# Optimization experiments

Hardware: AMD Instinct MI355X
Metric: run time of the kernel (lower is better)

Reference implementation:

```python
import jax, jax.numpy as jnp
import numpy as np

B, N, C, H = 8, 1024, 512, 8
EPS = 1e-6


def setup_inputs() -> dict:
    key = jax.random.key(0)
    k0, k1, k2, k3, k4 = jax.random.split(key, 5)
    x = jax.random.normal(k0, (B, N, C), dtype=jnp.float32)
    # nonnegative random-walk visit-frequency mask stand-in
    mask = jax.random.uniform(k1, (N, N), dtype=jnp.float32)
    w_qkv = jax.random.normal(k2, (C, 3 * C), dtype=jnp.float32) * 0.02
    w_out = jax.random.normal(k3, (C, C), dtype=jnp.float32) * 0.02
    b_out = jax.random.normal(k4, (C,), dtype=jnp.float32) * 0.02
    return {"x": x, "mask": mask, "w_qkv": w_qkv, "w_out": w_out, "b_out": b_out}


def reference(x, mask, w_qkv, w_out, b_out):
    b, n, c = x.shape
    d = c // H
    qkv = x @ w_qkv                                   # [B,N,3C]
    q, k, v = jnp.split(qkv, 3, axis=-1)

    def to_heads(t):
        return t.reshape(b, n, H, d).transpose(0, 2, 1, 3)  # [B,H,N,D]

    q, k, v = to_heads(q), to_heads(k), to_heads(v)
    # positive feature map
    q = jax.nn.relu(q) + EPS
    k = jax.nn.relu(k) + EPS
    # graph diffusion: (q^T @ mask)^T == einsum over source node m
    q = q + 0.1 * jnp.einsum('bhmd,mn->bhnd', q, mask)
    k = k + 0.1 * jnp.einsum('bhmd,mn->bhnd', k, mask)
    # linear kernel scores, elementwise-masked
    kernel = jnp.einsum('bhnd,bhmd->bhnm', q, k) * mask   # [B,H,N,N]
    z = 1.0 / (kernel.sum(axis=-1, keepdims=True) + EPS)  # [B,H,N,1]
    out = jnp.einsum('bhnm,bhmd->bhnd', kernel, v) * z    # [B,H,N,D]
    out = out.transpose(0, 2, 1, 3).reshape(b, n, c)      # [B,N,C]
    return out @ w_out + b_out
```

## Files before the change

### kernel.cpp

```cpp
#include <hip/hip_runtime.h>
#include <cstddef>

#define Bsz 8
#define Nn  1024
#define Cc  512
#define Hh  8
#define Dd  64
#define EPSF 1e-6f

typedef __attribute__((ext_vector_type(8))) short short8;
typedef __attribute__((ext_vector_type(4))) float floatx4;

static __device__ __forceinline__ short f2bf(float f) {
    union { float f; unsigned u; } v; v.f = f;
    unsigned r = (v.u + 0x7FFFu + ((v.u >> 16) & 1u)) >> 16;
    return (short)r;
}
static __device__ __forceinline__ float bf2f(short s) {
    union { unsigned u; float f; } v; v.u = ((unsigned)(unsigned short)s) << 16;
    return v.f;
}

#define GLOAD_LDS16(gp, lp)                                              \
    __builtin_amdgcn_global_load_lds(                                    \
        (const __attribute__((address_space(1))) void*)(gp),             \
        (__attribute__((address_space(3))) void*)(lp), 16, 0, 0)

static __device__ __forceinline__
void stage_tile(short* __restrict__ lds, const short* __restrict__ src,
                int ldsrc, int tid, int CHUNKS, int SLOTS) {
    #pragma unroll
    for (int s = tid; s < SLOTS; s += 256) {
        int r = s / CHUNKS, cs = s % CHUNKS;
        int gc = cs ^ (r & 7);
        GLOAD_LDS16(&src[(size_t)r * ldsrc + gc * 8], &lds[s * 8]);
    }
}
static __device__ __forceinline__
short8 fragT(const short* __restrict__ lds, int CHUNKS, int r, int lc) {
    return *(const short8*)&lds[(r * CHUNKS + (lc ^ (r & 7))) * 8];
}

#define FENCE() asm volatile("" ::: "memory")
#define BARRIER_RAW() do { FENCE(); __builtin_amdgcn_s_barrier(); FENCE(); } while (0)
#define WAITVM(N) asm volatile("s_waitcnt vmcnt(" #N ")" ::: "memory")

__global__ __launch_bounds__(256)
void prep_all(const float* __restrict__ x, const float* __restrict__ mask,
              const float* __restrict__ wq, const float* __restrict__ wo,
              short* __restrict__ xb, short* __restrict__ Ad,
              short* __restrict__ wqT, short* __restrict__ woT,
              short* __restrict__ mbf) {
    __shared__ float t[64][65];
    const int tid = threadIdx.x;
    const int bid = blockIdx.x;

    if (bid < 2048) {
        int idx = bid * 256 + tid;
        const float* s = &x[(size_t)idx * 8];
        union { short h[8]; int4 v; } u;
        #pragma unroll
        for (int j = 0; j < 8; j++) u.h[j] = f2bf(s[j]);
        *(int4*)&xb[(size_t)idx * 8] = u.v;
        return;
    }
    if (bid < 2304) {
        int idx = bid - 2048;
        const int n0 = (idx & 15) * 64, m0 = (idx >> 4) * 64;
        #pragma unroll
        for (int i = 0; i < 4; i++) {
            int k = i * 256 + tid;
            int r = k >> 4, c4 = (k & 15) * 4;
            *(float4*)&t[r][c4] = *(const float4*)&mask[(size_t)(m0 + r) * Nn + n0 + c4];
        }
        __syncthreads();
        #pragma unroll
        for (int i = 0; i < 4; i++) {
            int k = i * 256 + tid;
            int rr = k >> 4, c4 = (k & 15) * 4;
            union { short h[4]; int2 v; } u;
            #pragma unroll
            for (int j = 0; j < 4; j++) {
                int mm = c4 + j;
                float v = 0.1f * t[mm][rr] + ((n0 + rr) == (m0 + mm) ? 1.0f : 0.0f);
                u.h[j] = f2bf(v);
            }
            *(int2*)&Ad[(size_t)(n0 + rr) * Nn + m0 + c4] = u.v;
        }
        return;
    }
    if (bid < 2496) {
        int idx = bid - 2304;
        const int n0 = (idx % 24) * 64, k0 = (idx / 24) * 64;
        #pragma unroll
        for (int i = 0; i < 4; i++) {
            int k = i * 256 + tid;
            int r = k >> 4, c4 = (k & 15) * 4;
            *(float4*)&t[r][c4] = *(const float4*)&wq[(size_t)(k0 + r) * 1536 + n0 + c4];
        }
        __syncthreads();
        #pragma unroll
        for (int i = 0; i < 4; i++) {
            int k = i * 256 + tid;
            int rr = k >> 4, c4 = (k & 15) * 4;
            union { short h[4]; int2 v; } u;
            #pragma unroll
            for (int j = 0; j < 4; j++) u.h[j] = f2bf(t[c4 + j][rr]);
            *(int2*)&wqT[(size_t)(n0 + rr) * 512 + k0 + c4] = u.v;
        }
        return;
    }
    if (bid < 2560) {
        int idx = bid - 2496;
        const int n0 = (idx & 7) * 64, k0 = (idx >> 3) * 64;
        #pragma unroll
        for (int i = 0; i < 4; i++) {
            int k = i * 256 + tid;
            int r = k >> 4, c4 = (k & 15) * 4;
            *(float4*)&t[r][c4] = *(const float4*)&wo[(size_t)(k0 + r) * 512 + n0 + c4];
        }
        __syncthreads();
        #pragma unroll
        for (int i = 0; i < 4; i++) {
            int k = i * 256 + tid;
            int rr = k >> 4, c4 = (k & 15) * 4;
            union { short h[4]; int2 v; } u;
            #pragma unroll
            for (int j = 0; j < 4; j++) u.h[j] = f2bf(t[c4 + j][rr]);
            *(int2*)&woT[(size_t)(n0 + rr) * 512 + k0 + c4] = u.v;
        }
        return;
    }
    {
        int idx = (bid - 2560) * 256 + tid;
        const float* s = &mask[(size_t)idx * 8];
        union { short h[8]; int4 v; } u;
        #pragma unroll
        for (int j = 0; j < 8; j++) u.h[j] = f2bf(s[j]);
        *(int4*)&mbf[(size_t)idx * 8] = u.v;
    }
}

static __device__ __forceinline__
void stageA_half(short* __restrict__ buf, const short* __restrict__ gA,
                 int kt, int h, int tid) {
    #pragma unroll
    for (int kk = 0; kk < 2; kk++) {
        int i = tid + kk * 512;
        int run = i >> 9;
        int within = i & 511;
        int r = run * 128 + h * 64 + (within >> 3);
        int c = within & 7;
        int gc = c ^ (r & 7);
        GLOAD_LDS16(gA + (size_t)r * 512 + kt + gc * 8, buf + (r * 8 + c) * 8);
    }
}
static __device__ __forceinline__
void stageB_half(short* __restrict__ buf, const short* __restrict__ gB,
                 int kt, int h, int tid) {
    #pragma unroll
    for (int kk = 0; kk < 2; kk++) {
        int i = tid + kk * 512;
        int run = i >> 8;
        int within = i & 255;
        int r = run * 64 + h * 32 + (within >> 3);
        int c = within & 7;
        int gc = c ^ (r & 7);
        GLOAD_LDS16(gB + (size_t)r * 512 + kt + gc * 8, buf + (r * 8 + c) * 8);
    }
}

template<int MH>
static __device__ __forceinline__
void readA8(const short* __restrict__ bufA, short8 (&aF)[4][2],
            int wr, int l16, int quad) {
    #pragma unroll
    for (int f = 0; f < 4; f++)
        #pragma unroll
        for (int kk = 0; kk < 2; kk++)
            aF[f][kk] = fragT(bufA, 8, wr * 128 + MH * 64 + f * 16 + l16, kk * 4 + quad);
}
template<int NH>
static __device__ __forceinline__
void readB4(const short* __restrict__ bufB, short8 (&bF)[2][2],
            int wc, int l16, int quad) {
    #pragma unroll
    for (int g = 0; g < 2; g++)
        #pragma unroll
        for (int kk = 0; kk < 2; kk++)
            bF[g][kk] = fragT(bufB, 8, wc * 64 + NH * 32 + g * 16 + l16, kk * 4 + quad);
}
template<int MH, int NH>
static __device__ __forceinline__
void mfma16(short8 (&aF)[4][2], short8 (&bF)[2][2], floatx4 (&acc)[8][4]) {
    #pragma unroll
    for (int kk = 0; kk < 2; kk++)
        #pragma unroll
        for (int f = 0; f < 4; f++)
            #pragma unroll
            for (int g = 0; g < 2; g++)
                acc[MH * 4 + f][NH * 2 + g] = __builtin_amdgcn_mfma_f32_16x16x32_bf16(
                    aF[f][kk], bF[g][kk], acc[MH * 4 + f][NH * 2 + g], 0, 0, 0);
}

__global__ __launch_bounds__(512, 2)
void gemm_qkv(const short* __restrict__ xb, const short* __restrict__ wqT,
              short* __restrict__ qT, short* __restrict__ kT,
              short* __restrict__ vT) {
    extern __shared__ short smem[];

    const int tid = threadIdx.x;
    const int lin = blockIdx.x;
    const int wgid = (lin & 7) * 24 + (lin >> 3);
    const int mt = wgid / 6, nt = wgid % 6;
    const int m0 = mt * 256, n0 = nt * 256;

    const int wid = tid >> 6, lane = tid & 63;
    const int quad = lane >> 4, l16 = lane & 15;
    const int wr = wid >> 2, wc = wid & 3;

    const short* Ab = xb  + (size_t)m0 * 512;
    const short* Bb = wqT + (size_t)n0 * 512;

    floatx4 acc[8][4];
    #pragma unroll
    for (int i = 0; i < 8; i++)
        #pragma unroll
        for (int j = 0; j < 4; j++) acc[i][j] = (floatx4){0.f, 0.f, 0.f, 0.f};

    short8 aF[4][2], bF[2][2];

    stageA_half(smem,          Ab, 0, 0, tid);
    stageB_half(smem + 16384,  Bb, 0, 0, tid);
    stageA_half(smem,          Ab, 0, 1, tid);
    stageB_half(smem + 16384,  Bb, 0, 1, tid);
    WAITVM(4); BARRIER_RAW();

    for (int j = 0; j < 8; ++j) {
        const short* cA = smem + (j & 1) * 32768;
        const short* cB = cA + 16384;
        short* nA = smem + ((j + 1) & 1) * 32768;
        short* nB = nA + 16384;
        const int kn = ((j + 1) & 7) * 64;

        readA8<0>(cA, aF, wr, l16, quad);
        readB4<0>(cB, bF, wc, l16, quad);
        stageA_half(nA, Ab, kn, 0, tid);
        stageB_half(nB, Bb, kn, 0, tid);
        BARRIER_RAW();
        __builtin_amdgcn_s_setprio(1);
        mfma16<0, 0>(aF, bF, acc);
        __builtin_amdgcn_s_setprio(0);
        WAITVM(4); BARRIER_RAW();

        readA8<1>(cA, aF, wr, l16, quad);
        stageA_half(nA, Ab, kn, 1, tid);
        stageB_half(nB, Bb, kn, 1, tid);
        BARRIER_RAW();
        __builtin_amdgcn_s_setprio(1);
        mfma16<1, 0>(aF, bF, acc);
        __builtin_amdgcn_s_setprio(0);
        BARRIER_RAW();

        readB4<1>(cB, bF, wc, l16, quad);
        BARRIER_RAW();
        __builtin_amdgcn_s_setprio(1);
        mfma16<1, 1>(aF, bF, acc);
        __builtin_amdgcn_s_setprio(0);
        BARRIER_RAW();

        readA8<0>(cA, aF, wr, l16, quad);
        BARRIER_RAW();
        __builtin_amdgcn_s_setprio(1);
        mfma16<0, 1>(aF, bF, acc);
        __builtin_amdgcn_s_setprio(0);
        WAITVM(4); BARRIER_RAW();
    }

    WAITVM(0); BARRIER_RAW();

    short* T = smem + wid * 8192;
    const int doRelu = (n0 < 1024);
    #pragma unroll
    for (int mf = 0; mf < 8; mf++)
        #pragma unroll
        for (int nf = 0; nf < 4; nf++)
            #pragma unroll
            for (int rr = 0; rr < 4; rr++) {
                float v = acc[mf][nf][rr];
                if (doRelu) v = fmaxf(v, 0.0f) + EPSF;
                int row = nf * 16 + l16;
                int col = mf * 16 + quad * 4 + rr;
                T[row * 128 + (col ^ ((row & 15) << 3))] = f2bf(v);
            }
    const int gm0 = m0 + wr * 128;
    const int b = gm0 >> 10, m_in0 = gm0 & 1023;
    #pragma unroll
    for (int g = 0; g < 4; g++) {
        int row = (lane >> 2) + g * 16;
        int gn = n0 + wc * 64 + row;
        int part = gn >> 9, ci = gn & 511;
        short* base = (part == 0) ? qT : (part == 1) ? kT : vT;
        short* dst = base + ((size_t)b * 512 + ci) * 1024 + m_in0;
        #pragma unroll
        for (int cc = 0; cc < 4; cc++) {
            int cs = ((lane & 3) + cc * 4) * 8;
            *(int4*)&dst[cs] = *(const int4*)&T[row * 128 + (cs ^ ((row & 15) << 3))];
        }
    }
}

static __device__ __forceinline__
void dstageA_half(short* __restrict__ buf, const short* __restrict__ gA,
                  int kt, int h, int tid) {
    #pragma unroll
    for (int kk = 0; kk < 2; kk++) {
        int i = tid + kk * 512;
        int rl = i >> 3;
        int c  = i & 7;
        int r  = (rl >> 5) * 64 + h * 32 + (rl & 31);
        int gc = c ^ (r & 7);
        GLOAD_LDS16(gA + (size_t)r * 1024 + kt + gc * 8, buf + (r * 8 + c) * 8);
    }
}
static __device__ __forceinline__
void dstageB_half(short* __restrict__ buf, const short* __restrict__ gB,
                  int kt, int h, int tid) {
    int rl = tid >> 3;
    int c  = tid & 7;
    int r  = (rl >> 5) * 64 + h * 32 + (rl & 31);
    int gc = c ^ (r & 7);
    GLOAD_LDS16(gB + (size_t)r * 1024 + kt + gc * 8, buf + (r * 8 + c) * 8);
}
template<int MH>
static __device__ __forceinline__
void dreadA(const short* __restrict__ bufA, short8 (&aF)[2][2],
            int wr, int l16, int quad) {
    #pragma unroll
    for (int f = 0; f < 2; f++)
        #pragma unroll
        for (int kk = 0; kk < 2; kk++)
            aF[f][kk] = fragT(bufA, 8, wr * 64 + MH * 32 + f * 16 + l16, kk * 4 + quad);
}
template<int NH>
static __device__ __forceinline__
void dreadB(const short* __restrict__ bufB, short8 (&bF)[2][2],
            int wc, int l16, int quad) {
    #pragma unroll
    for (int g = 0; g < 2; g++)
        #pragma unroll
        for (int kk = 0; kk < 2; kk++)
            bF[g][kk] = fragT(bufB, 8, wc * 64 + NH * 32 + g * 16 + l16, kk * 4 + quad);
}
template<int MH, int NH>
static __device__ __forceinline__
void dmfma8(short8 (&aF)[2][2], short8 (&bF)[2][2], floatx4 (&acc)[4][4]) {
    #pragma unroll
    for (int kk = 0; kk < 2; kk++)
        #pragma unroll
        for (int f = 0; f < 2; f++)
            #pragma unroll
            for (int g = 0; g < 2; g++)
                acc[MH * 2 + f][NH * 2 + g] = __builtin_amdgcn_mfma_f32_16x16x32_bf16(
                    aF[f][kk], bF[g][kk], acc[MH * 2 + f][NH * 2 + g], 0, 0, 0);
}

__global__ __launch_bounds__(512, 2)
void gemm_diff8(const short* __restrict__ Ad, const short* __restrict__ qT,
                const short* __restrict__ kT, short* __restrict__ qd,
                short* __restrict__ kd) {
    extern __shared__ short smem[];

    const int tid = threadIdx.x;
    const int lin = blockIdx.x;
    const int wgid = (lin & 7) * 32 + (lin >> 3);
    const int mt = wgid >> 6, ct = wgid & 63;
    const int m0 = mt * 256;
    const int seg = ct >> 2, cb = (ct & 3) * 128;
    const int b = seg >> 1, part = seg & 1;

    const short* Bb = ((part ? kT : qT) + (size_t)b * 512 * 1024) + (size_t)cb * 1024;
    short* outb = (part ? kd : qd) + (size_t)b * 1024 * 512;
    const short* Abase = Ad + (size_t)m0 * 1024;

    const int wid = tid >> 6, lane = tid & 63;
    const int quad = lane >> 4, l16 = lane & 15;
    const int wr = wid >> 1, wc = wid & 1;

    floatx4 acc[4][4];
    #pragma unroll
    for (int i = 0; i < 4; i++)
        #pragma unroll
        for (int j = 0; j < 4; j++) acc[i][j] = (floatx4){0.f, 0.f, 0.f, 0.f};

    short8 aF[2][2], bF[2][2];

    dstageA_half(smem,          Abase, 0, 0, tid);
    dstageB_half(smem + 16384,  Bb,    0, 0, tid);
    dstageA_half(smem,          Abase, 0, 1, tid);
    dstageB_half(smem + 16384,  Bb,    0, 1, tid);
    WAITVM(3); BARRIER_RAW();

    for (int j = 0; j < 16; ++j) {
        const short* cA = smem + (j & 1) * 24576;
        const short* cB = cA + 16384;
        short* nA = smem + ((j + 1) & 1) * 24576;
        short* nB = nA + 16384;
        const int kn = ((j + 1) & 15) * 64;

        dreadA<0>(cA, aF, wr, l16, quad);
        dreadB<0>(cB, bF, wc, l16, quad);
        dstageA_half(nA, Abase, kn, 0, tid);
        dstageB_half(nB, Bb,    kn, 0, tid);
        BARRIER_RAW();
        __builtin_amdgcn_s_setprio(1);
        dmfma8<0, 0>(aF, bF, acc);
        __builtin_amdgcn_s_setprio(0);
        WAITVM(3); BARRIER_RAW();

        dreadA<1>(cA, aF, wr, l16, quad);
        dstageA_half(nA, Abase, kn, 1, tid);
        dstageB_half(nB, Bb,    kn, 1, tid);
        BARRIER_RAW();
        __builtin_amdgcn_s_setprio(1);
        dmfma8<1, 0>(aF, bF, acc);
        __builtin_amdgcn_s_setprio(0);
        BARRIER_RAW();

        dreadB<1>(cB, bF, wc, l16, quad);
        BARRIER_RAW();
        __builtin_amdgcn_s_setprio(1);
        dmfma8<1, 1>(aF, bF, acc);
        __builtin_amdgcn_s_setprio(0);
        BARRIER_RAW();

        dreadA<0>(cA, aF, wr, l16, quad);
        BARRIER_RAW();
        __builtin_amdgcn_s_setprio(1);
        dmfma8<0, 1>(aF, bF, acc);
        __builtin_amdgcn_s_setprio(0);
        WAITVM(3); BARRIER_RAW();
    }
    WAITVM(0);

    #pragma unroll
    for (int fr = 0; fr < 4; fr++)
        #pragma unroll
        for (int rr = 0; rr < 4; rr++) {
            int n = m0 + wr * 64 + fr * 16 + quad * 4 + rr;
            #pragma unroll
            for (int fc = 0; fc < 4; fc++) {
                int c = cb + wc * 64 + fc * 16 + l16;
                outb[(size_t)n * 512 + c] = f2bf(acc[fr][fc][rr]);
            }
        }
}

static __device__ __forceinline__
void attn_tile(const short* __restrict__ ks, const short* __restrict__ vt,
               short* __restrict__ ss, const int2 (&M)[2][4],
               const short8 (&aT)[2][2], float (&dreg)[2],
               floatx4 (&nacc)[2][4], int wave, int quad, int l16) {
    const int ssrow[2] = { wave * 32 + l16, wave * 32 + 16 + l16 };
    #pragma unroll
    for (int mt = 0; mt < 4; mt++) {
        const short8 k0f = fragT(ks, 8, mt * 16 + l16, quad);
        const short8 k1f = fragT(ks, 8, mt * 16 + l16, 4 + quad);
        #pragma unroll
        for (int t = 0; t < 2; t++) {
            floatx4 s = (floatx4){0.f, 0.f, 0.f, 0.f};
            s = __builtin_amdgcn_mfma_f32_16x16x32_bf16(k0f, aT[t][0], s, 0, 0, 0);
            s = __builtin_amdgcn_mfma_f32_16x16x32_bf16(k1f, aT[t][1], s, 0, 0, 0);
            const int row = ssrow[t];
            const int c = mt * 16 + quad * 4;
            const int off = (row * 8 + ((c >> 3) ^ (row & 7))) * 8 + (c & 7);
            union { short hh[4]; int2 v; } mk; mk.v = M[t][mt];
            float sv0 = s[0] * bf2f(mk.hh[0]);
            float sv1 = s[1] * bf2f(mk.hh[1]);
            float sv2 = s[2] * bf2f(mk.hh[2]);
            float sv3 = s[3] * bf2f(mk.hh[3]);
            dreg[t] += (sv0 + sv1) + (sv2 + sv3);
            int lo, hi;
            asm("v_cvt_pk_bf16_f32 %0, %1, %2" : "=v"(lo) : "v"(sv0), "v"(sv1));
            asm("v_cvt_pk_bf16_f32 %0, %1, %2" : "=v"(hi) : "v"(sv2), "v"(sv3));
            int2 pv; pv.x = lo; pv.y = hi;
            *(int2*)&ss[off] = pv;
        }
    }
    short8 p[2][2];
    #pragma unroll
    for (int t = 0; t < 2; t++) {
        p[t][0] = fragT(ss, 8, wave * 32 + t * 16 + l16, quad);
        p[t][1] = fragT(ss, 8, wave * 32 + t * 16 + l16, 4 + quad);
    }
    __builtin_amdgcn_s_setprio(1);
    #pragma unroll
    for (int dt = 0; dt < 4; dt++) {
        const short8 v0 = fragT(vt, 8, dt * 16 + l16, quad);
        const short8 v1 = fragT(vt, 8, dt * 16 + l16, 4 + quad);
        #pragma unroll
        for (int t = 0; t < 2; t++) {
            nacc[t][dt] = __builtin_amdgcn_mfma_f32_16x16x32_bf16(p[t][0], v0, nacc[t][dt], 0, 0, 0);
            nacc[t][dt] = __builtin_amdgcn_mfma_f32_16x16x32_bf16(p[t][1], v1, nacc[t][dt], 0, 0, 0);
        }
    }
    __builtin_amdgcn_s_setprio(0);
}

__global__ __launch_bounds__(256)
void attn_mfma(const short* __restrict__ qd, const short* __restrict__ kd,
               const short* __restrict__ vTg, const short* __restrict__ mbf,
               short* __restrict__ abf) {
    __shared__ short qss[8192];
    __shared__ short kv[2][8192];

    const int tid = threadIdx.x;
    const int bh = blockIdx.x;
    const int b = bh >> 3, h = bh & 7;
    const int n0 = blockIdx.y * 128;

    const int wave = tid >> 6, lane = tid & 63;
    const int quad = lane >> 4, l16 = lane & 15;

    const short* Qb = qd + ((size_t)b * Nn + n0) * Cc + h * Dd;
    const short* Kb = kd + (size_t)b * Nn * Cc + h * Dd;
    const short* Vb = vTg + ((size_t)b * Cc + h * Dd) * Nn;
    const short* baseM = mbf + (size_t)(n0 + wave * 32 + l16) * Nn + quad * 4;

    stage_tile(qss, Qb, Cc, tid, 8, 1024);
    stage_tile(kv[0],        Kb, Cc, tid, 8, 512);
    stage_tile(kv[0] + 4096, Vb, Nn, tid, 8, 512);
    int2 Ma[2][4], Mb2[2][4];
    #pragma unroll
    for (int t = 0; t < 2; t++)
        #pragma unroll
        for (int mt = 0; mt < 4; mt++)
            Ma[t][mt] = *(const int2*)(baseM + t * 16 * Nn + mt * 16);
    WAITVM(0); BARRIER_RAW();

    short8 aT[2][2];
    #pragma unroll
    for (int t = 0; t < 2; t++) {
        aT[t][0] = fragT(qss, 8, wave * 32 + t * 16 + l16, quad);
        aT[t][1] = fragT(qss, 8, wave * 32 + t * 16 + l16, 4 + quad);
    }

    float dreg[2] = {0.f, 0.f};
    floatx4 nacc[2][4];
    #pragma unroll
    for (int t = 0; t < 2; t++)
        #pragma unroll
        for (int i = 0; i < 4; i++) nacc[t][i] = (floatx4){0.f, 0.f, 0.f, 0.f};

    for (int jo = 0; jo < 8; jo++) {
        const int j0 = jo * 2;
        stage_tile(kv[1],        Kb + (size_t)(j0 + 1) * 64 * Cc, Cc, tid, 8, 512);
        stage_tile(kv[1] + 4096, Vb + (j0 + 1) * 64,              Nn, tid, 8, 512);
        #pragma unroll
        for (int t = 0; t < 2; t++)
            #pragma unroll
            for (int mt = 0; mt < 4; mt++)
                Mb2[t][mt] = *(const int2*)(baseM + t * 16 * Nn + (j0 + 1) * 64 + mt * 16);
        attn_tile(kv[0], kv[0] + 4096, qss, Ma, aT, dreg, nacc, wave, quad, l16);
        WAITVM(0); BARRIER_RAW();

        if (jo < 7) {
            stage_tile(kv[0],        Kb + (size_t)(j0 + 2) * 64 * Cc, Cc, tid, 8, 512);
            stage_tile(kv[0] + 4096, Vb + (j0 + 2) * 64,              Nn, tid, 8, 512);
            #pragma unroll
            for (int t = 0; t < 2; t++)
                #pragma unroll
                for (int mt = 0; mt < 4; mt++)
                    Ma[t][mt] = *(const int2*)(baseM + t * 16 * Nn + (j0 + 2) * 64 + mt * 16);
        }
        attn_tile(kv[1], kv[1] + 4096, qss, Mb2, aT, dreg, nacc, wave, quad, l16);
        WAITVM(0); BARRIER_RAW();
    }

    #pragma unroll
    for (int t = 0; t < 2; t++) {
        dreg[t] += __shfl_xor(dreg[t], 16, 64);
        dreg[t] += __shfl_xor(dreg[t], 32, 64);
    }

    #pragma unroll
    for (int t = 0; t < 2; t++)
        #pragma unroll
        for (int r = 0; r < 4; r++) {
            int nloc = quad * 4 + r;
            float den = __shfl(dreg[t], nloc, 64);
            int n = n0 + wave * 32 + t * 16 + nloc;
            float zr = 1.0f / (den + EPSF);
            #pragma unroll
            for (int dt = 0; dt < 4; dt++) {
                size_t o = ((size_t)b * Nn + n) * Cc + h * Dd + dt * 16 + l16;
                abf[o] = f2bf(nacc[t][dt][r] * zr);
            }
        }
}

__global__ __launch_bounds__(256)
void gemm_out(const short* __restrict__ abf, const short* __restrict__ woT,
              const float* __restrict__ bias, float* __restrict__ out) {
    __shared__ short smem[12288];
    short* As = smem;
    short* Bs = smem + 4096;

    const int tid = threadIdx.x;
    const int m0 = blockIdx.y * 64;
    const int n0 = blockIdx.x * 128;
    const int wave = tid >> 6, lane = tid & 63;
    const int quad = lane >> 4, l16 = lane & 15;
    const int wm = (wave >> 1) * 32, wn = (wave & 1) * 64;

    floatx4 acc[2][4];
    #pragma unroll
    for (int i = 0; i < 2; i++)
        #pragma unroll
        for (int j = 0; j < 4; j++) acc[i][j] = (floatx4){0.f, 0.f, 0.f, 0.f};

    const short* Ab = abf + (size_t)m0 * 512;
    const short* Bb = woT + (size_t)n0 * 512;

    for (int k0 = 0; k0 < 512; k0 += 64) {
        __syncthreads();
        stage_tile(As, Ab + k0, 512, tid, 8, 512);
        stage_tile(Bs, Bb + k0, 512, tid, 8, 1024);
        __syncthreads();
        #pragma unroll
        for (int kh = 0; kh < 2; kh++) {
            short8 a[2], b[4];
            #pragma unroll
            for (int i = 0; i < 2; i++)
                a[i] = fragT(As, 8, wm + i * 16 + l16, kh * 4 + quad);
            #pragma unroll
            for (int i = 0; i < 4; i++)
                b[i] = fragT(Bs, 8, wn + i * 16 + l16, kh * 4 + quad);
            #pragma unroll
            for (int mi = 0; mi < 2; mi++)
                #pragma unroll
                for (int ni = 0; ni < 4; ni++)
                    acc[mi][ni] = __builtin_amdgcn_mfma_f32_16x16x32_bf16(
                        a[mi], b[ni], acc[mi][ni], 0, 0, 0);
        }
    }

    #pragma unroll
    for (int mi = 0; mi < 2; mi++)
        #pragma unroll
        for (int r = 0; r < 4; r++) {
            int m = m0 + wm + mi * 16 + quad * 4 + r;
            #pragma unroll
            for (int ni = 0; ni < 4; ni++) {
                int n = n0 + wn + ni * 16 + l16;
                out[(size_t)m * 512 + n] = acc[mi][ni][r] + bias[n];
            }
        }
}

extern "C" void kernel_launch(void* const* d_in, const int* in_sizes, int n_in,
                              void* d_out, int out_size, void* d_ws, size_t ws_size,
                              hipStream_t stream) {
    const float* x     = (const float*)d_in[0];
    const float* mask  = (const float*)d_in[1];
    const float* w_qkv = (const float*)d_in[2];
    const float* w_out = (const float*)d_in[3];
    const float* b_out = (const float*)d_in[4];
    float* out = (float*)d_out;

    char* p = (char*)d_ws;
    short* xb  = (short*)p; p += 8388608;
    short* wqT = (short*)p; p += 1572864;
    short* Ad  = (short*)p; p += 2097152;
    short* woT = (short*)p; p += 524288;
    short* mbf = (short*)p; p += 2097152;
    short* qT  = (short*)p; p += 8388608;
    short* kT  = (short*)p; p += 8388608;
    short* vT  = (short*)p; p += 8388608;
    short* qd  = (short*)p; p += 8388608;
    short* kd  = (short*)p; p += 8388608;
    short* abf = (short*)p; p += 8388608;

    static int attr_set = 0;
    if (!attr_set) {
        hipFuncSetAttribute(reinterpret_cast<const void*>(gemm_qkv),
                            hipFuncAttributeMaxDynamicSharedMemorySize, 131072);
        hipFuncSetAttribute(reinterpret_cast<const void*>(gemm_diff8),
                            hipFuncAttributeMaxDynamicSharedMemorySize, 98304);
        attr_set = 1;
    }

    dim3 blk(256);

    prep_all  <<<3072, blk, 0, stream>>>(x, mask, w_qkv, w_out,
                                         xb, Ad, wqT, woT, mbf);
    gemm_qkv  <<<dim3(192), dim3(512), 131072, stream>>>(xb, wqT, qT, kT, vT);
    gemm_diff8<<<dim3(256), dim3(512), 98304, stream>>>(Ad, qT, kT, qd, kd);
    attn_mfma <<<dim3(64, 8),  blk, 0, stream>>>(qd, kd, vT, mbf, abf);
    gemm_out  <<<dim3(4, 128), blk, 0, stream>>>(abf, woT, b_out, out);
}
```

Measured before the change: 174.4 us.

## Split attention key range across two wave groups per block and merge partials

```diff
diff --git a/kernel.cpp b/kernel.cpp
--- a/kernel.cpp
+++ b/kernel.cpp
@@ -44,6 +44,7 @@
 #define FENCE() asm volatile("" ::: "memory")
 #define BARRIER_RAW() do { FENCE(); __builtin_amdgcn_s_barrier(); FENCE(); } while (0)
 #define WAITVM(N) asm volatile("s_waitcnt vmcnt(" #N ")" ::: "memory")
+#define WAITLGKM0() asm volatile("s_waitcnt lgkmcnt(0)" ::: "memory")
 
 __global__ __launch_bounds__(256)
 void prep_all(const float* __restrict__ x, const float* __restrict__ mask,
@@ -457,11 +458,10 @@
 }
 
 static __device__ __forceinline__
-void attn_tile(const short* __restrict__ ks, const short* __restrict__ vt,
-               short* __restrict__ ss, const int2 (&M)[2][4],
-               const short8 (&aT)[2][2], float (&dreg)[2],
-               floatx4 (&nacc)[2][4], int wave, int quad, int l16) {
-    const int ssrow[2] = { wave * 32 + l16, wave * 32 + 16 + l16 };
+void attn_qk(const short* __restrict__ ks, short* __restrict__ pb,
+             const int2 (&M)[2][4], const short8 (&aT)[2][2],
+             float (&dreg)[2], int wloc, int quad, int l16) {
+    const int ssrow[2] = { wloc * 32 + l16, wloc * 32 + 16 + l16 };
     #pragma unroll
     for (int mt = 0; mt < 4; mt++) {
         const short8 k0f = fragT(ks, 8, mt * 16 + l16, quad);
@@ -484,14 +484,18 @@
             asm("v_cvt_pk_bf16_f32 %0, %1, %2" : "=v"(lo) : "v"(sv0), "v"(sv1));
             asm("v_cvt_pk_bf16_f32 %0, %1, %2" : "=v"(hi) : "v"(sv2), "v"(sv3));
             int2 pv; pv.x = lo; pv.y = hi;
-            *(int2*)&ss[off] = pv;
-        }
-    }
+            *(int2*)&pb[off] = pv;
+        }
+    }
+}
+static __device__ __forceinline__
+void attn_pv(const short* __restrict__ vt, const short* __restrict__ pb,
+             floatx4 (&nacc)[2][4], int wloc, int quad, int l16) {
     short8 p[2][2];
     #pragma unroll
     for (int t = 0; t < 2; t++) {
-        p[t][0] = fragT(ss, 8, wave * 32 + t * 16 + l16, quad);
-        p[t][1] = fragT(ss, 8, wave * 32 + t * 16 + l16, 4 + quad);
+        p[t][0] = fragT(pb, 8, wloc * 32 + t * 16 + l16, quad);
+        p[t][1] = fragT(pb, 8, wloc * 32 + t * 16 + l16, 4 + quad);
     }
     __builtin_amdgcn_s_setprio(1);
     #pragma unroll
@@ -507,43 +511,54 @@
     __builtin_amdgcn_s_setprio(0);
 }
 
-__global__ __launch_bounds__(256)
+__global__ __launch_bounds__(512, 4)
 void attn_mfma(const short* __restrict__ qd, const short* __restrict__ kd,
                const short* __restrict__ vTg, const short* __restrict__ mbf,
                short* __restrict__ abf) {
-    __shared__ short qss[8192];
-    __shared__ short kv[2][8192];
+    extern __shared__ short smem[];
+    short* qss = smem;
+    short* p1s = smem + 8192;
+    short* kv  = smem + 16384;
 
     const int tid = threadIdx.x;
     const int bh = blockIdx.x;
     const int b = bh >> 3, h = bh & 7;
     const int n0 = blockIdx.y * 128;
 
-    const int wave = tid >> 6, lane = tid & 63;
+    const int wid = tid >> 6, lane = tid & 63;
+    const int g = wid >> 2, wloc = wid & 3;
     const int quad = lane >> 4, l16 = lane & 15;
+    const int tid256 = tid & 255;
 
     const short* Qb = qd + ((size_t)b * Nn + n0) * Cc + h * Dd;
-    const short* Kb = kd + (size_t)b * Nn * Cc + h * Dd;
-    const short* Vb = vTg + ((size_t)b * Cc + h * Dd) * Nn;
-    const short* baseM = mbf + (size_t)(n0 + wave * 32 + l16) * Nn + quad * 4;
-
-    stage_tile(qss, Qb, Cc, tid, 8, 1024);
-    stage_tile(kv[0],        Kb, Cc, tid, 8, 512);
-    stage_tile(kv[0] + 4096, Vb, Nn, tid, 8, 512);
-    int2 Ma[2][4], Mb2[2][4];
+    const short* Kb = kd + (size_t)b * Nn * Cc + h * Dd + (size_t)(g * 512) * Cc;
+    const short* Vb = vTg + ((size_t)b * Cc + h * Dd) * Nn + g * 512;
+    const short* baseM = mbf + (size_t)(n0 + wloc * 32 + l16) * Nn + quad * 4 + g * 512;
+
+    short* Ks = kv + g * 8192;
+    short* Vs = Ks + 4096;
+    short* pb = g ? p1s : qss;
+
+    if (tid < 256) stage_tile(qss, Qb, Cc, tid, 8, 1024);
+    stage_tile(Ks, Kb, Cc, tid256, 8, 512);
+    int2 M[2][4];
     #pragma unroll
     for (int t = 0; t < 2; t++)
         #pragma unroll
         for (int mt = 0; mt < 4; mt++)
-            Ma[t][mt] = *(const int2*)(baseM + t * 16 * Nn + mt * 16);
-    WAITVM(0); BARRIER_RAW();
+            M[t][mt] = *(const int2*)(baseM + t * 16 * Nn + mt * 16);
+    stage_tile(Vs, Vb, Nn, tid256, 8, 512);
+    WAITVM(2); BARRIER_RAW();
 
     short8 aT[2][2];
     #pragma unroll
     for (int t = 0; t < 2; t++) {
-        aT[t][0] = fragT(qss, 8, wave * 32 + t * 16 + l16, quad);
-        aT[t][1] = fragT(qss, 8, wave * 32 + t * 16 + l16, 4 + quad);
-    }
+        aT[t][0] = fragT(qss, 8, wloc * 32 + t * 16 + l16, quad);
+        aT[t][1] = fragT(qss, 8, wloc * 32 + t * 16 + l16, 4 + quad);
+    }
+    WAITLGKM0();
+    __builtin_amdgcn_sched_barrier(0);
+    BARRIER_RAW();
 
     float dreg[2] = {0.f, 0.f};
     floatx4 nacc[2][4];
@@ -552,29 +567,22 @@
         #pragma unroll
         for (int i = 0; i < 4; i++) nacc[t][i] = (floatx4){0.f, 0.f, 0.f, 0.f};
 
-    for (int jo = 0; jo < 8; jo++) {
-        const int j0 = jo * 2;
-        stage_tile(kv[1],        Kb + (size_t)(j0 + 1) * 64 * Cc, Cc, tid, 8, 512);
-        stage_tile(kv[1] + 4096, Vb + (j0 + 1) * 64,              Nn, tid, 8, 512);
-        #pragma unroll
-        for (int t = 0; t < 2; t++)
-            #pragma unroll
-            for (int mt = 0; mt < 4; mt++)
-                Mb2[t][mt] = *(const int2*)(baseM + t * 16 * Nn + (j0 + 1) * 64 + mt * 16);
-        attn_tile(kv[0], kv[0] + 4096, qss, Ma, aT, dreg, nacc, wave, quad, l16);
+    for (int j = 0; j < 8; j++) {
+        attn_qk(Ks, pb, M, aT, dreg, wloc, quad, l16);
         WAITVM(0); BARRIER_RAW();
 
-        if (jo < 7) {
-            stage_tile(kv[0],        Kb + (size_t)(j0 + 2) * 64 * Cc, Cc, tid, 8, 512);
-            stage_tile(kv[0] + 4096, Vb + (j0 + 2) * 64,              Nn, tid, 8, 512);
+        if (j < 7) {
+            stage_tile(Ks, Kb + (size_t)(j + 1) * 64 * Cc, Cc, tid256, 8, 512);
             #pragma unroll
             for (int t = 0; t < 2; t++)
                 #pragma unroll
                 for (int mt = 0; mt < 4; mt++)
-                    Ma[t][mt] = *(const int2*)(baseM + t * 16 * Nn + (j0 + 2) * 64 + mt * 16);
-        }
-        attn_tile(kv[1], kv[1] + 4096, qss, Mb2, aT, dreg, nacc, wave, quad, l16);
-        WAITVM(0); BARRIER_RAW();
+                    M[t][mt] = *(const int2*)(baseM + t * 16 * Nn + (j + 1) * 64 + mt * 16);
+        }
+        attn_pv(Vs, pb, nacc, wloc, quad, l16);
+        BARRIER_RAW();
+        if (j < 7) stage_tile(Vs, Vb + (j + 1) * 64, Nn, tid256, 8, 512);
+        WAITVM(2); BARRIER_RAW();
     }
 
     #pragma unroll
@@ -582,21 +590,48 @@
         dreg[t] += __shfl_xor(dreg[t], 16, 64);
         dreg[t] += __shfl_xor(dreg[t], 32, 64);
     }
-
-    #pragma unroll
-    for (int t = 0; t < 2; t++)
-        #pragma unroll
-        for (int r = 0; r < 4; r++) {
-            int nloc = quad * 4 + r;
-            float den = __shfl(dreg[t], nloc, 64);
-            int n = n0 + wave * 32 + t * 16 + nloc;
-            float zr = 1.0f / (den + EPSF);
-            #pragma unroll
-            for (int dt = 0; dt < 4; dt++) {
-                size_t o = ((size_t)b * Nn + n) * Cc + h * Dd + dt * 16 + l16;
-                abf[o] = f2bf(nacc[t][dt][r] * zr);
+    float* mrg  = (float*)kv;
+    float* den1 = (float*)qss;
+    if (g == 1) {
+        #pragma unroll
+        for (int t = 0; t < 2; t++) {
+            #pragma unroll
+            for (int dt = 0; dt < 4; dt++)
+                #pragma unroll
+                for (int r = 0; r < 4; r++)
+                    mrg[(wloc * 32 + t * 16 + quad * 4 + r) * 64 + dt * 16 + l16] =
+                        nacc[t][dt][r];
+            if (lane < 16) den1[wloc * 32 + t * 16 + l16] = dreg[t];
+        }
+    }
+    WAITLGKM0();
+    BARRIER_RAW();
+    if (g == 0) {
+        #pragma unroll
+        for (int t = 0; t < 2; t++) {
+            dreg[t] += den1[wloc * 32 + t * 16 + l16];
+            #pragma unroll
+            for (int dt = 0; dt < 4; dt++)
+                #pragma unroll
+                for (int r = 0; r < 4; r++)
+                    nacc[t][dt][r] +=
+                        mrg[(wloc * 32 + t * 16 + quad * 4 + r) * 64 + dt * 16 + l16];
+        }
+        #pragma unroll
+        for (int t = 0; t < 2; t++)
+            #pragma unroll
+            for (int r = 0; r < 4; r++) {
+                int nloc = quad * 4 + r;
+                float den = __shfl(dreg[t], nloc, 64);
+                int n = n0 + wloc * 32 + t * 16 + nloc;
+                float zr = 1.0f / (den + EPSF);
+                #pragma unroll
+                for (int dt = 0; dt < 4; dt++) {
+                    size_t o = ((size_t)b * Nn + n) * Cc + h * Dd + dt * 16 + l16;
+                    abf[o] = f2bf(nacc[t][dt][r] * zr);
+                }
             }
-        }
+    }
 }
 
 __global__ __launch_bounds__(256)
@@ -687,6 +722,8 @@
                             hipFuncAttributeMaxDynamicSharedMemorySize, 131072);
         hipFuncSetAttribute(reinterpret_cast<const void*>(gemm_diff8),
                             hipFuncAttributeMaxDynamicSharedMemorySize, 98304);
+        hipFuncSetAttribute(reinterpret_cast<const void*>(attn_mfma),
+                            hipFuncAttributeMaxDynamicSharedMemorySize, 65536);
         attr_set = 1;
     }
 
@@ -696,6 +733,6 @@
                                          xb, Ad, wqT, woT, mbf);
     gemm_qkv  <<<dim3(192), dim3(512), 131072, stream>>>(xb, wqT, qT, kT, vT);
     gemm_diff8<<<dim3(256), dim3(512), 98304, stream>>>(Ad, qT, kT, qd, kd);
-    attn_mfma <<<dim3(64, 8),  blk, 0, stream>>>(qd, kd, vT, mbf, abf);
+    attn_mfma <<<dim3(64, 8), dim3(512), 65536, stream>>>(qd, kd, vT, mbf, abf);
     gemm_out  <<<dim3(4, 128), blk, 0, stream>>>(abf, woT, b_out, out);
 }
```

Result: slower. 180.6 us (+3.5%).
